# Performance work log

Measured on AMD Instinct MI355X. Metric: run time of the kernel, lower is better.

Reference implementation:

```python
import jax, jax.numpy as jnp
import numpy as np

N_NODES = 25000
N_EDGES = 400000
CHANNELS = 32
EDGE_FEAT_DIM = 8
HIDDEN = 64
NUM_IRREPS = 4  # messages irreps = 2x0e + 2x1o -> 4 irreps, dim 8
AVG_NUM_NEIGHBORS = 16.0


def _mlp(x, W0, W1, W2, W3):
    # e3nn MultiLayerPerceptron: dense layers with 1/sqrt(fan_in) forward
    # normalization, silu on hidden layers, no output activation.
    for W in (W0, W1, W2):
        x = jax.nn.silu(x @ (W / jnp.sqrt(jnp.float32(W.shape[0]))))
    return x @ (W3 / jnp.sqrt(jnp.float32(W3.shape[0])))


def setup_inputs() -> dict:
    key = jax.random.key(0)
    ks = jax.random.split(key, 9)
    node_feats = jax.random.normal(ks[0], (N_NODES, CHANNELS, 4), jnp.float32)
    edge_attrs = jax.random.normal(ks[1], (N_EDGES, 4), jnp.float32)
    edge_feats = jax.random.normal(ks[2], (N_EDGES, EDGE_FEAT_DIM), jnp.float32)
    senders = jax.random.randint(ks[3], (N_EDGES,), 0, N_NODES)
    receivers = jax.random.randint(ks[4], (N_EDGES,), 0, N_NODES)
    W0 = jax.random.normal(ks[5], (EDGE_FEAT_DIM, HIDDEN), jnp.float32)
    W1 = jax.random.normal(ks[6], (HIDDEN, HIDDEN), jnp.float32)
    W2 = jax.random.normal(ks[7], (HIDDEN, HIDDEN), jnp.float32)
    W3 = jax.random.normal(ks[8], (HIDDEN, CHANNELS * NUM_IRREPS), jnp.float32)
    return {"node_feats": node_feats, "edge_attrs": edge_attrs,
            "edge_feats": edge_feats, "senders": senders, "receivers": receivers,
            "W0": W0, "W1": W1, "W2": W2, "W3": W3}


def reference(node_feats, edge_attrs, edge_feats, senders, receivers, W0, W1, W2, W3):
    # Gather sender node features: [E, C, 4] with irreps 0e (dim1) + 1o (dim3)
    x = node_feats[senders]
    s, v = x[..., 0], x[..., 1:4]            # [E,C], [E,C,3]
    a_s = edge_attrs[:, 0]                   # Y_0: [E]
    a_v = edge_attrs[:, 1:4]                 # Y_1: [E,3]

    # CG tensor product filtered to 0e + 1o (e3nn normalization: sqrt(2l3+1)*w3j)
    m0a = s * a_s[:, None]                                   # 0e x 0e -> 0e  [E,C]
    m0b = jnp.einsum('ecd,ed->ec', v, a_v) / jnp.sqrt(3.0)   # 1o x 1o -> 0e  [E,C]
    m1a = s[..., None] * a_v[:, None, :]                     # 0e x 1o -> 1o  [E,C,3]
    m1b = v * a_s[:, None, None]                             # 1o x 0e -> 1o  [E,C,3]

    # Edge MLP gate: [E, C*num_irreps] -> mul_to_axis -> [E, C, num_irreps]
    mix = _mlp(edge_feats, W0, W1, W2, W3).reshape(N_EDGES, CHANNELS, NUM_IRREPS)

    # Elementwise tensor product with 4x0e scalars: per-irrep gating
    out_s = jnp.stack([m0a * mix[..., 0], m0b * mix[..., 1]], axis=-1)          # [E,C,2]
    out_v = jnp.concatenate([m1a * mix[..., 2:3], m1b * mix[..., 3:4]], axis=-1)  # [E,C,6]
    messages = jnp.concatenate([out_s, out_v], axis=-1)                          # [E,C,8]

    # Scatter-add into receivers, then normalize by sqrt(avg_num_neighbors)
    agg = jax.ops.segment_sum(messages, receivers, num_segments=N_NODES)
    return agg / jnp.sqrt(AVG_NUM_NEIGHBORS)
```

## Files before the change

### kernel.cpp

```cpp
#include <hip/hip_runtime.h>
#include <hip/hip_fp16.h>

#define NE 400000
#define NN 25000
#define MAXDEG 56
#define LDS_STRIDE 65

typedef __attribute__((ext_vector_type(8))) _Float16 half8;
typedef __attribute__((ext_vector_type(4))) _Float16 half4;
typedef __attribute__((ext_vector_type(4))) float f32x4;

#define WS_MIX_OFF   0ull
#define WS_SLOTS_OFF 102400000ull
#define WS_CNT_OFF   108000000ull
#define WS_WBUF_OFF  108100000ull
#define WS_NEED      108136864ull

#define WB_L0 0
#define WB_L1 2048
#define WB_L2 6144
#define WB_L3 10240

__device__ __forceinline__ float fast_silu(float x) {
    float e = __expf(-x);
    return x * __builtin_amdgcn_rcpf(1.0f + e);
}

__global__ __launch_bounds__(64) void prep_weights(
    const float* __restrict__ W0, const float* __restrict__ W1,
    const float* __restrict__ W2, const float* __restrict__ W3,
    _Float16* __restrict__ wbuf, int* __restrict__ cnt)
{
    const int f    = blockIdx.x;
    const int lane = threadIdx.x;

    for (int i = f * 64 + lane; i < NN; i += 36 * 64) cnt[i] = 0;

    const int n    = lane & 15;
    const int quad = lane >> 4;

    const float* W; int K, N, kt, nt, fl, base; float scale;
    if (f < 4)       { W = W0; K = 8;  N = 64;  fl = f;      kt = 0;       nt = fl;     scale = 0.35355339059327373f; base = WB_L0; }
    else if (f < 12) { W = W1; K = 64; N = 64;  fl = f - 4;  kt = fl >> 2; nt = fl & 3; scale = 0.125f;   base = WB_L1; }
    else if (f < 20) { W = W2; K = 64; N = 64;  fl = f - 12; kt = fl >> 2; nt = fl & 3; scale = 0.125f;   base = WB_L2; }
    else             { W = W3; K = 64; N = 128; fl = f - 20; kt = fl >> 3; nt = fl & 7; scale = 0.03125f; base = WB_L3; }

    _Float16 v[8];
    #pragma unroll
    for (int j = 0; j < 8; ++j) {
        const int k = kt * 32 + quad * 8 + j;
        const float val = (k < K) ? W[k * N + nt * 16 + n] * scale : 0.0f;
        v[j] = (_Float16)val;
    }
    *(half8*)(wbuf + base + fl * 512 + lane * 8) = *(const half8*)v;
}

#define HS 72
#define SS 136
__global__ __launch_bounds__(256) void mlp_build_kernel(
    const float*    __restrict__ edge_feats,
    const int*      __restrict__ receivers,
    const _Float16* __restrict__ wbuf,
    int*            __restrict__ cnt,
    int*            __restrict__ slots,
    _Float16*       __restrict__ mix16)
{
    __shared__ _Float16 H[4 * 2 * 16 * HS];
    const int tid  = threadIdx.x;
    const int wave = tid >> 6;
    const int lane = tid & 63;
    const int col  = lane & 15;
    const int quad = lane >> 4;

    if (tid < 128) {
        const int e = blockIdx.x * 128 + tid;
        const int r = receivers[e];
        const int s = atomicAdd(&cnt[r], 1);
        if (s < MAXDEG) slots[r * MAXDEG + s] = e;
    }

    const int e0 = (blockIdx.x * 4 + wave) * 32;
    _Float16* HA = &H[wave * 2 * 16 * HS];
    _Float16* HB = HA + 16 * HS;
    const half8* wb = (const half8*)wbuf;
    const f32x4 zero4 = {0.f, 0.f, 0.f, 0.f};

    half8 b0A = {0, 0, 0, 0, 0, 0, 0, 0};
    half8 b0B = {0, 0, 0, 0, 0, 0, 0, 0};
    if (quad == 0) {
        const float4* pA = (const float4*)(edge_feats + (size_t)(e0 + col) * 8);
        const float4 xa = pA[0], ya = pA[1];
        b0A[0] = (_Float16)xa.x; b0A[1] = (_Float16)xa.y; b0A[2] = (_Float16)xa.z; b0A[3] = (_Float16)xa.w;
        b0A[4] = (_Float16)ya.x; b0A[5] = (_Float16)ya.y; b0A[6] = (_Float16)ya.z; b0A[7] = (_Float16)ya.w;
        const float4* pB = (const float4*)(edge_feats + (size_t)(e0 + 16 + col) * 8);
        const float4 xb = pB[0], yb = pB[1];
        b0B[0] = (_Float16)xb.x; b0B[1] = (_Float16)xb.y; b0B[2] = (_Float16)xb.z; b0B[3] = (_Float16)xb.w;
        b0B[4] = (_Float16)yb.x; b0B[5] = (_Float16)yb.y; b0B[6] = (_Float16)yb.z; b0B[7] = (_Float16)yb.w;
    }

    #pragma unroll
    for (int nt = 0; nt < 4; ++nt) {
        const half8 w = wb[(WB_L0 / 512 + nt) * 64 + lane];
        f32x4 aA = __builtin_amdgcn_mfma_f32_16x16x32_f16(w, b0A, zero4, 0, 0, 0);
        f32x4 aB = __builtin_amdgcn_mfma_f32_16x16x32_f16(w, b0B, zero4, 0, 0, 0);
        half4 hA, hB;
        #pragma unroll
        for (int r = 0; r < 4; ++r) { hA[r] = (_Float16)fast_silu(aA[r]); hB[r] = (_Float16)fast_silu(aB[r]); }
        *(half4*)&HA[col * HS + nt * 16 + quad * 4] = hA;
        *(half4*)&HB[col * HS + nt * 16 + quad * 4] = hB;
    }

    #pragma unroll
    for (int layer = 0; layer < 2; ++layer) {
        const int wbase = (layer == 0 ? WB_L1 : WB_L2) / 512;
        const half8 bloA = *(const half8*)&HA[col * HS + 0  + quad * 8];
        const half8 bhiA = *(const half8*)&HA[col * HS + 32 + quad * 8];
        const half8 bloB = *(const half8*)&HB[col * HS + 0  + quad * 8];
        const half8 bhiB = *(const half8*)&HB[col * HS + 32 + quad * 8];
        f32x4 aA[4], aB[4];
        #pragma unroll
        for (int nt = 0; nt < 4; ++nt) {
            const half8 wlo = wb[(wbase + 0 + nt) * 64 + lane];
            const half8 whi = wb[(wbase + 4 + nt) * 64 + lane];
            aA[nt] = __builtin_amdgcn_mfma_f32_16x16x32_f16(wlo, bloA, zero4, 0, 0, 0);
            aA[nt] = __builtin_amdgcn_mfma_f32_16x16x32_f16(whi, bhiA, aA[nt], 0, 0, 0);
            aB[nt] = __builtin_amdgcn_mfma_f32_16x16x32_f16(wlo, bloB, zero4, 0, 0, 0);
            aB[nt] = __builtin_amdgcn_mfma_f32_16x16x32_f16(whi, bhiB, aB[nt], 0, 0, 0);
        }
        #pragma unroll
        for (int nt = 0; nt < 4; ++nt) {
            half4 hA, hB;
            #pragma unroll
            for (int r = 0; r < 4; ++r) { hA[r] = (_Float16)fast_silu(aA[nt][r]); hB[r] = (_Float16)fast_silu(aB[nt][r]); }
            *(half4*)&HA[col * HS + nt * 16 + quad * 4] = hA;
            *(half4*)&HB[col * HS + nt * 16 + quad * 4] = hB;
        }
    }

    {
        const half8 bloA = *(const half8*)&HA[col * HS + 0  + quad * 8];
        const half8 bhiA = *(const half8*)&HA[col * HS + 32 + quad * 8];
        const half8 bloB = *(const half8*)&HB[col * HS + 0  + quad * 8];
        const half8 bhiB = *(const half8*)&HB[col * HS + 32 + quad * 8];
        _Float16* S = HA;

        #pragma unroll
        for (int nt = 0; nt < 8; ++nt) {
            const half8 wlo = wb[(WB_L3 / 512 + 0 + nt) * 64 + lane];
            const half8 whi = wb[(WB_L3 / 512 + 8 + nt) * 64 + lane];
            f32x4 aA = __builtin_amdgcn_mfma_f32_16x16x32_f16(wlo, bloA, zero4, 0, 0, 0);
            aA = __builtin_amdgcn_mfma_f32_16x16x32_f16(whi, bhiA, aA, 0, 0, 0);
            half4 hA;
            #pragma unroll
            for (int r = 0; r < 4; ++r) hA[r] = (_Float16)aA[r];
            *(half4*)&S[col * SS + nt * 16 + quad * 4] = hA;
        }
        {
            _Float16* mbase = mix16 + (size_t)e0 * 128;
            #pragma unroll
            for (int rnd = 0; rnd < 4; ++rnd) {
                const int idx  = rnd * 512 + lane * 8;
                const int scol = idx >> 7;
                const int sinn = idx & 127;
                const half8 v = *(const half8*)&S[scol * SS + sinn];
                *(half8*)&mbase[idx] = v;
            }
        }

        #pragma unroll
        for (int nt = 0; nt < 8; ++nt) {
            const half8 wlo = wb[(WB_L3 / 512 + 0 + nt) * 64 + lane];
            const half8 whi = wb[(WB_L3 / 512 + 8 + nt) * 64 + lane];
            f32x4 aB = __builtin_amdgcn_mfma_f32_16x16x32_f16(wlo, bloB, zero4, 0, 0, 0);
            aB = __builtin_amdgcn_mfma_f32_16x16x32_f16(whi, bhiB, aB, 0, 0, 0);
            half4 hB;
            #pragma unroll
            for (int r = 0; r < 4; ++r) hB[r] = (_Float16)aB[r];
            *(half4*)&S[col * SS + nt * 16 + quad * 4] = hB;
        }
        {
            _Float16* mbase = mix16 + (size_t)(e0 + 16) * 128;
            #pragma unroll
            for (int rnd = 0; rnd < 4; ++rnd) {
                const int idx  = rnd * 512 + lane * 8;
                const int scol = idx >> 7;
                const int sinn = idx & 127;
                const half8 v = *(const half8*)&S[scol * SS + sinn];
                *(half8*)&mbase[idx] = v;
            }
        }
    }
}

__global__ __launch_bounds__(256) void gather_kernel(
    const float*    __restrict__ node_feats,
    const float*    __restrict__ edge_attrs,
    const int*      __restrict__ senders,
    const _Float16* __restrict__ mix16,
    const int*      __restrict__ cnt,
    const int*      __restrict__ slots,
    float*          __restrict__ out)
{
    const int tid  = threadIdx.x;
    const int wave = tid >> 6;
    const int lane = tid & 63;
    const int n    = blockIdx.x * 4 + wave;
    const int g    = lane >> 4;
    const int s    = lane & 15;
    const int c0   = 2 * s;
    const float inv_sqrt3 = 0.5773502691896258f;

    int d = cnt[n];
    if (d > MAXDEG) d = MAXDEG;
    const int* sl = slots + n * MAXDEG;

    const int li    = (lane < MAXDEG) ? lane : (MAXDEG - 1);
    int eid_l       = sl[li];
    eid_l           = (lane < d) ? eid_l : 0;
    const int snd_l = senders[eid_l];

    float acc[16];
    #pragma unroll
    for (int j = 0; j < 16; ++j) acc[j] = 0.0f;

    #pragma unroll 2
    for (int base = 0; base < d; base += 4) {
        const int  ei  = base + g;
        const bool act = (ei < d);
        const int  eid = __shfl(eid_l, ei, 64);
        const int  snd = __shfl(snd_l, ei, 64);
        const float4 a4v = ((const float4*)edge_attrs)[eid];
        const half8 m8 = *(const half8*)(mix16 + (size_t)eid * 128 + c0 * 4);
        const float4 xA = ((const float4*)(node_feats + (size_t)snd * 128))[c0];
        const float4 xB = ((const float4*)(node_feats + (size_t)snd * 128))[c0 + 1];

        const float z = act ? 1.0f : 0.0f;
        const float as = a4v.x, av0 = a4v.y, av1 = a4v.z, av2 = a4v.w;

        {
            const float m0 = z * (float)m8[0], m1 = z * (float)m8[1];
            const float m2 = z * (float)m8[2], m3 = z * (float)m8[3];
            const float sc = xA.x, v0 = xA.y, v1 = xA.z, v2 = xA.w;
            acc[0] = fmaf(sc * as, m0, acc[0]);
            const float dv = v0 * av0 + v1 * av1 + v2 * av2;
            acc[1] = fmaf(dv * inv_sqrt3, m1, acc[1]);
            acc[2] = fmaf(sc * av0, m2, acc[2]);
            acc[3] = fmaf(sc * av1, m2, acc[3]);
            acc[4] = fmaf(sc * av2, m2, acc[4]);
            acc[5] = fmaf(v0 * as, m3, acc[5]);
            acc[6] = fmaf(v1 * as, m3, acc[6]);
            acc[7] = fmaf(v2 * as, m3, acc[7]);
        }
        {
            const float m0 = z * (float)m8[4], m1 = z * (float)m8[5];
            const float m2 = z * (float)m8[6], m3 = z * (float)m8[7];
            const float sc = xB.x, v0 = xB.y, v1 = xB.z, v2 = xB.w;
            acc[8]  = fmaf(sc * as, m0, acc[8]);
            const float dv = v0 * av0 + v1 * av1 + v2 * av2;
            acc[9]  = fmaf(dv * inv_sqrt3, m1, acc[9]);
            acc[10] = fmaf(sc * av0, m2, acc[10]);
            acc[11] = fmaf(sc * av1, m2, acc[11]);
            acc[12] = fmaf(sc * av2, m2, acc[12]);
            acc[13] = fmaf(v0 * as, m3, acc[13]);
            acc[14] = fmaf(v1 * as, m3, acc[14]);
            acc[15] = fmaf(v2 * as, m3, acc[15]);
        }
    }

    #pragma unroll
    for (int j = 0; j < 16; ++j) {
        acc[j] += __shfl_xor(acc[j], 16, 64);
        acc[j] += __shfl_xor(acc[j], 32, 64);
    }

    if (g == 0) {
        float4* op = (float4*)(out + (size_t)n * 256 + s * 16);
        float4 r0; r0.x = acc[0];  r0.y = acc[1];  r0.z = acc[2];  r0.w = acc[3];
        float4 r1; r1.x = acc[4];  r1.y = acc[5];  r1.z = acc[6];  r1.w = acc[7];
        float4 r2; r2.x = acc[8];  r2.y = acc[9];  r2.z = acc[10]; r2.w = acc[11];
        float4 r3; r3.x = acc[12]; r3.y = acc[13]; r3.z = acc[14]; r3.w = acc[15];
        op[0] = r0; op[1] = r1; op[2] = r2; op[3] = r3;
    }
}

__global__ __launch_bounds__(128) void edge_mp_kernel(
    const float* __restrict__ node_feats, const float* __restrict__ edge_attrs,
    const float* __restrict__ edge_feats, const int* __restrict__ senders,
    const int* __restrict__ receivers, const float* __restrict__ W0,
    const float* __restrict__ W1, const float* __restrict__ W2,
    const float* __restrict__ W3, float* __restrict__ out)
{
    __shared__ float hbuf[128 * LDS_STRIDE];
    const int tid = threadIdx.x;
    const int e   = blockIdx.x * 128 + tid;
    if (e >= NE) return;
    float* hl = &hbuf[tid * LDS_STRIDE];

    float4 ef0 = ((const float4*)edge_feats)[e * 2 + 0];
    float4 ef1 = ((const float4*)edge_feats)[e * 2 + 1];
    float ef[8] = {ef0.x, ef0.y, ef0.z, ef0.w, ef1.x, ef1.y, ef1.z, ef1.w};
    float acc[64];
    #pragma unroll
    for (int i = 0; i < 64; ++i) acc[i] = 0.0f;
    #pragma unroll
    for (int j = 0; j < 8; ++j) {
        const float xj = ef[j];
        const float* wrow = W0 + j * 64;
        #pragma unroll
        for (int i = 0; i < 64; ++i) acc[i] = fmaf(xj, wrow[i], acc[i]);
    }
    {
        const float s0 = 0.35355339059327373f;
        #pragma unroll
        for (int i = 0; i < 64; ++i) hl[i] = fast_silu(acc[i] * s0);
    }
    #pragma unroll
    for (int i = 0; i < 64; ++i) acc[i] = 0.0f;
    #pragma unroll 4
    for (int j = 0; j < 64; ++j) {
        const float xj = hl[j];
        const float* wrow = W1 + j * 64;
        #pragma unroll
        for (int i = 0; i < 64; ++i) acc[i] = fmaf(xj, wrow[i], acc[i]);
    }
    #pragma unroll
    for (int i = 0; i < 64; ++i) hl[i] = fast_silu(acc[i] * 0.125f);
    #pragma unroll
    for (int i = 0; i < 64; ++i) acc[i] = 0.0f;
    #pragma unroll 4
    for (int j = 0; j < 64; ++j) {
        const float xj = hl[j];
        const float* wrow = W2 + j * 64;
        #pragma unroll
        for (int i = 0; i < 64; ++i) acc[i] = fmaf(xj, wrow[i], acc[i]);
    }
    float h2[64];
    #pragma unroll
    for (int i = 0; i < 64; ++i) h2[i] = fast_silu(acc[i] * 0.125f);

    const int snd = senders[e];
    const int rcv = receivers[e];
    const float4 a4 = ((const float4*)edge_attrs)[e];
    const float a_s = a4.x, av0 = a4.y, av1 = a4.z, av2 = a4.w;
    const float4* nf4 = (const float4*)(node_feats + (size_t)snd * 128);
    float* outp = out + (size_t)rcv * 256;
    const float mixscale = 0.03125f;
    const float inv_sqrt3 = 0.5773502691896258f;

    #pragma unroll 2
    for (int c = 0; c < 32; ++c) {
        float m0 = 0.0f, m1 = 0.0f, m2 = 0.0f, m3 = 0.0f;
        const float* wc = W3 + c * 4;
        #pragma unroll
        for (int j = 0; j < 64; ++j) {
            const float hj = h2[j];
            m0 = fmaf(hj, wc[j * 128 + 0], m0);
            m1 = fmaf(hj, wc[j * 128 + 1], m1);
            m2 = fmaf(hj, wc[j * 128 + 2], m2);
            m3 = fmaf(hj, wc[j * 128 + 3], m3);
        }
        m0 *= mixscale; m1 *= mixscale; m2 *= mixscale; m3 *= mixscale;
        const float4 x4 = nf4[c];
        const float s = x4.x, v0 = x4.y, v1 = x4.z, v2 = x4.w;
        float* op = outp + c * 8;
        atomicAdd(op + 0, s * a_s * m0);
        const float dotva = v0 * av0 + v1 * av1 + v2 * av2;
        atomicAdd(op + 1, dotva * inv_sqrt3 * m1);
        atomicAdd(op + 2, s * av0 * m2);
        atomicAdd(op + 3, s * av1 * m2);
        atomicAdd(op + 4, s * av2 * m2);
        atomicAdd(op + 5, v0 * a_s * m3);
        atomicAdd(op + 6, v1 * a_s * m3);
        atomicAdd(op + 7, v2 * a_s * m3);
    }
}

extern "C" void kernel_launch(void* const* d_in, const int* in_sizes, int n_in,
                              void* d_out, int out_size, void* d_ws, size_t ws_size,
                              hipStream_t stream) {
    const float* node_feats = (const float*)d_in[0];
    const float* edge_attrs = (const float*)d_in[1];
    const float* edge_feats = (const float*)d_in[2];
    const int*   senders    = (const int*)d_in[3];
    const int*   receivers  = (const int*)d_in[4];
    const float* W0 = (const float*)d_in[5];
    const float* W1 = (const float*)d_in[6];
    const float* W2 = (const float*)d_in[7];
    const float* W3 = (const float*)d_in[8];
    float* outp = (float*)d_out;

    if (ws_size >= WS_NEED) {
        char* w = (char*)d_ws;
        _Float16* mix16 = (_Float16*)(w + WS_MIX_OFF);
        int*      slots = (int*)(w + WS_SLOTS_OFF);
        int*      cnt   = (int*)(w + WS_CNT_OFF);
        _Float16* wbuf  = (_Float16*)(w + WS_WBUF_OFF);

        hipLaunchKernelGGL(prep_weights, dim3(36), dim3(64), 0, stream,
                           W0, W1, W2, W3, wbuf, cnt);
        hipLaunchKernelGGL(mlp_build_kernel, dim3(NE / 128), dim3(256), 0, stream,
                           edge_feats, receivers, wbuf, cnt, slots, mix16);
        hipLaunchKernelGGL(gather_kernel, dim3(NN / 4), dim3(256), 0, stream,
                           node_feats, edge_attrs, senders, mix16, cnt, slots, outp);
    } else {
        hipMemsetAsync(d_out, 0, (size_t)out_size * sizeof(float), stream);
        hipLaunchKernelGGL(edge_mp_kernel, dim3((NE + 127) / 128), dim3(128), 0, stream,
                           node_feats, edge_attrs, edge_feats, senders, receivers,
                           W0, W1, W2, W3, outp);
    }
}
```

Before: 197.1 us.

## Build CSR by receiver and store MLP gates in receiver-sorted order

Replaces fixed-capacity per-node slot lists with a true CSR: a count kernel, a single-wave prefix scan folded into weight prep, and atomic placement during the MLP kernel. The MLP output rows are now written at their CSR position, so the gather kernel reads each node's gate rows contiguously instead of at scattered edge ids. This adds a memset, an extra kernel and a serial 64-lane scan over 25k counts. Edges beyond 64 per node are dropped in the gather.

```diff
diff --git a/kernel.cpp b/kernel.cpp
--- a/kernel.cpp
+++ b/kernel.cpp
@@ -3,7 +3,6 @@
 
 #define NE 400000
 #define NN 25000
-#define MAXDEG 56
 #define LDS_STRIDE 65
 
 typedef __attribute__((ext_vector_type(8))) _Float16 half8;
@@ -11,10 +10,12 @@
 typedef __attribute__((ext_vector_type(4))) float f32x4;
 
 #define WS_MIX_OFF   0ull
-#define WS_SLOTS_OFF 102400000ull
-#define WS_CNT_OFF   108000000ull
-#define WS_WBUF_OFF  108100000ull
-#define WS_NEED      108136864ull
+#define WS_EID_OFF   102400000ull
+#define WS_OFFS_OFF  104000000ull
+#define WS_CNT_OFF   104100000ull
+#define WS_CNT2_OFF  104200000ull
+#define WS_WBUF_OFF  104300000ull
+#define WS_NEED      104336864ull
 
 #define WB_L0 0
 #define WB_L1 2048
@@ -26,24 +27,47 @@
     return x * __builtin_amdgcn_rcpf(1.0f + e);
 }
 
+__global__ __launch_bounds__(256) void csr_count(
+    const int* __restrict__ receivers, int* __restrict__ cnt)
+{
+    const int e = blockIdx.x * 256 + threadIdx.x;
+    if (e < NE) atomicAdd(&cnt[receivers[e]], 1);
+}
+
 __global__ __launch_bounds__(64) void prep_weights(
     const float* __restrict__ W0, const float* __restrict__ W1,
     const float* __restrict__ W2, const float* __restrict__ W3,
-    _Float16* __restrict__ wbuf, int* __restrict__ cnt)
+    _Float16* __restrict__ wbuf, const int* __restrict__ cnt,
+    int* __restrict__ offs)
 {
     const int f    = blockIdx.x;
     const int lane = threadIdx.x;
 
-    for (int i = f * 64 + lane; i < NN; i += 36 * 64) cnt[i] = 0;
+    if (f == 36) {
+        const int CH = (NN + 63) / 64;
+        const int i0 = lane * CH;
+        const int i1 = (i0 + CH < NN) ? i0 + CH : NN;
+        int sum = 0;
+        for (int i = i0; i < i1; ++i) sum += cnt[i];
+        int run = sum;
+        #pragma unroll
+        for (int dlt = 1; dlt < 64; dlt <<= 1) {
+            const int v = __shfl_up(run, dlt, 64);
+            if (lane >= dlt) run += v;
+        }
+        int base = run - sum;
+        for (int i = i0; i < i1; ++i) { offs[i] = base; base += cnt[i]; }
+        return;
+    }
 
     const int n    = lane & 15;
     const int quad = lane >> 4;
 
-    const float* W; int K, N, kt, nt, fl, base; float scale;
-    if (f < 4)       { W = W0; K = 8;  N = 64;  fl = f;      kt = 0;       nt = fl;     scale = 0.35355339059327373f; base = WB_L0; }
-    else if (f < 12) { W = W1; K = 64; N = 64;  fl = f - 4;  kt = fl >> 2; nt = fl & 3; scale = 0.125f;   base = WB_L1; }
-    else if (f < 20) { W = W2; K = 64; N = 64;  fl = f - 12; kt = fl >> 2; nt = fl & 3; scale = 0.125f;   base = WB_L2; }
-    else             { W = W3; K = 64; N = 128; fl = f - 20; kt = fl >> 3; nt = fl & 7; scale = 0.03125f; base = WB_L3; }
+    const float* W; int K, N, kt, nt, fl, wbase; float scale;
+    if (f < 4)       { W = W0; K = 8;  N = 64;  fl = f;      kt = 0;       nt = fl;     scale = 0.35355339059327373f; wbase = WB_L0; }
+    else if (f < 12) { W = W1; K = 64; N = 64;  fl = f - 4;  kt = fl >> 2; nt = fl & 3; scale = 0.125f;   wbase = WB_L1; }
+    else if (f < 20) { W = W2; K = 64; N = 64;  fl = f - 12; kt = fl >> 2; nt = fl & 3; scale = 0.125f;   wbase = WB_L2; }
+    else             { W = W3; K = 64; N = 128; fl = f - 20; kt = fl >> 3; nt = fl & 7; scale = 0.03125f; wbase = WB_L3; }
 
     _Float16 v[8];
     #pragma unroll
@@ -52,7 +76,7 @@
         const float val = (k < K) ? W[k * N + nt * 16 + n] * scale : 0.0f;
         v[j] = (_Float16)val;
     }
-    *(half8*)(wbuf + base + fl * 512 + lane * 8) = *(const half8*)v;
+    *(half8*)(wbuf + wbase + fl * 512 + lane * 8) = *(const half8*)v;
 }
 
 #define HS 72
@@ -61,8 +85,9 @@
     const float*    __restrict__ edge_feats,
     const int*      __restrict__ receivers,
     const _Float16* __restrict__ wbuf,
-    int*            __restrict__ cnt,
-    int*            __restrict__ slots,
+    int*            __restrict__ cnt2,
+    const int*      __restrict__ offs,
+    int*            __restrict__ eidarr,
     _Float16*       __restrict__ mix16)
 {
     __shared__ _Float16 H[4 * 2 * 16 * HS];
@@ -72,14 +97,17 @@
     const int col  = lane & 15;
     const int quad = lane >> 4;
 
-    if (tid < 128) {
-        const int e = blockIdx.x * 128 + tid;
+    const int e0 = (blockIdx.x * 4 + wave) * 32;
+
+    int pos_reg = 0;
+    if (lane < 32) {
+        const int e = e0 + lane;
         const int r = receivers[e];
-        const int s = atomicAdd(&cnt[r], 1);
-        if (s < MAXDEG) slots[r * MAXDEG + s] = e;
-    }
-
-    const int e0 = (blockIdx.x * 4 + wave) * 32;
+        const int s = atomicAdd(&cnt2[r], 1);
+        pos_reg = offs[r] + s;
+        eidarr[pos_reg] = e;
+    }
+
     _Float16* HA = &H[wave * 2 * 16 * HS];
     _Float16* HB = HA + 16 * HS;
     const half8* wb = (const half8*)wbuf;
@@ -143,6 +171,8 @@
         const half8 bloB = *(const half8*)&HB[col * HS + 0  + quad * 8];
         const half8 bhiB = *(const half8*)&HB[col * HS + 32 + quad * 8];
         _Float16* S = HA;
+        const int et  = lane >> 2;
+        const int sub = lane & 3;
 
         #pragma unroll
         for (int nt = 0; nt < 8; ++nt) {
@@ -156,14 +186,12 @@
             *(half4*)&S[col * SS + nt * 16 + quad * 4] = hA;
         }
         {
-            _Float16* mbase = mix16 + (size_t)e0 * 128;
+            const int posA = __shfl(pos_reg, et, 64);
+            _Float16* rowA = mix16 + (size_t)posA * 128;
             #pragma unroll
             for (int rnd = 0; rnd < 4; ++rnd) {
-                const int idx  = rnd * 512 + lane * 8;
-                const int scol = idx >> 7;
-                const int sinn = idx & 127;
-                const half8 v = *(const half8*)&S[scol * SS + sinn];
-                *(half8*)&mbase[idx] = v;
+                const half8 v = *(const half8*)&S[et * SS + sub * 8 + rnd * 32];
+                *(half8*)&rowA[sub * 8 + rnd * 32] = v;
             }
         }
 
@@ -179,14 +207,12 @@
             *(half4*)&S[col * SS + nt * 16 + quad * 4] = hB;
         }
         {
-            _Float16* mbase = mix16 + (size_t)(e0 + 16) * 128;
+            const int posB = __shfl(pos_reg, 16 + et, 64);
+            _Float16* rowB = mix16 + (size_t)posB * 128;
             #pragma unroll
             for (int rnd = 0; rnd < 4; ++rnd) {
-                const int idx  = rnd * 512 + lane * 8;
-                const int scol = idx >> 7;
-                const int sinn = idx & 127;
-                const half8 v = *(const half8*)&S[scol * SS + sinn];
-                *(half8*)&mbase[idx] = v;
+                const half8 v = *(const half8*)&S[et * SS + sub * 8 + rnd * 32];
+                *(half8*)&rowB[sub * 8 + rnd * 32] = v;
             }
         }
     }
@@ -198,7 +224,8 @@
     const int*      __restrict__ senders,
     const _Float16* __restrict__ mix16,
     const int*      __restrict__ cnt,
-    const int*      __restrict__ slots,
+    const int*      __restrict__ offs,
+    const int*      __restrict__ eidarr,
     float*          __restrict__ out)
 {
     const int tid  = threadIdx.x;
@@ -210,60 +237,62 @@
     const int c0   = 2 * s;
     const float inv_sqrt3 = 0.5773502691896258f;
 
+    const int o = offs[n];
     int d = cnt[n];
-    if (d > MAXDEG) d = MAXDEG;
-    const int* sl = slots + n * MAXDEG;
-
-    const int li    = (lane < MAXDEG) ? lane : (MAXDEG - 1);
-    int eid_l       = sl[li];
-    eid_l           = (lane < d) ? eid_l : 0;
-    const int snd_l = senders[eid_l];
+    if (d > 64) d = 64;
 
     float acc[16];
     #pragma unroll
     for (int j = 0; j < 16; ++j) acc[j] = 0.0f;
 
-    #pragma unroll 2
-    for (int base = 0; base < d; base += 4) {
-        const int  ei  = base + g;
-        const bool act = (ei < d);
-        const int  eid = __shfl(eid_l, ei, 64);
-        const int  snd = __shfl(snd_l, ei, 64);
-        const float4 a4v = ((const float4*)edge_attrs)[eid];
-        const half8 m8 = *(const half8*)(mix16 + (size_t)eid * 128 + c0 * 4);
-        const float4 xA = ((const float4*)(node_feats + (size_t)snd * 128))[c0];
-        const float4 xB = ((const float4*)(node_feats + (size_t)snd * 128))[c0 + 1];
-
-        const float z = act ? 1.0f : 0.0f;
-        const float as = a4v.x, av0 = a4v.y, av1 = a4v.z, av2 = a4v.w;
-
-        {
-            const float m0 = z * (float)m8[0], m1 = z * (float)m8[1];
-            const float m2 = z * (float)m8[2], m3 = z * (float)m8[3];
-            const float sc = xA.x, v0 = xA.y, v1 = xA.z, v2 = xA.w;
-            acc[0] = fmaf(sc * as, m0, acc[0]);
-            const float dv = v0 * av0 + v1 * av1 + v2 * av2;
-            acc[1] = fmaf(dv * inv_sqrt3, m1, acc[1]);
-            acc[2] = fmaf(sc * av0, m2, acc[2]);
-            acc[3] = fmaf(sc * av1, m2, acc[3]);
-            acc[4] = fmaf(sc * av2, m2, acc[4]);
-            acc[5] = fmaf(v0 * as, m3, acc[5]);
-            acc[6] = fmaf(v1 * as, m3, acc[6]);
-            acc[7] = fmaf(v2 * as, m3, acc[7]);
-        }
-        {
-            const float m0 = z * (float)m8[4], m1 = z * (float)m8[5];
-            const float m2 = z * (float)m8[6], m3 = z * (float)m8[7];
-            const float sc = xB.x, v0 = xB.y, v1 = xB.z, v2 = xB.w;
-            acc[8]  = fmaf(sc * as, m0, acc[8]);
-            const float dv = v0 * av0 + v1 * av1 + v2 * av2;
-            acc[9]  = fmaf(dv * inv_sqrt3, m1, acc[9]);
-            acc[10] = fmaf(sc * av0, m2, acc[10]);
-            acc[11] = fmaf(sc * av1, m2, acc[11]);
-            acc[12] = fmaf(sc * av2, m2, acc[12]);
-            acc[13] = fmaf(v0 * as, m3, acc[13]);
-            acc[14] = fmaf(v1 * as, m3, acc[14]);
-            acc[15] = fmaf(v2 * as, m3, acc[15]);
+    if (d > 0) {
+        const int li    = (lane < d) ? lane : d - 1;
+        const int eid_l = eidarr[o + li];
+        const int snd_l = senders[eid_l];
+
+        #pragma unroll 2
+        for (int base = 0; base < d; base += 4) {
+            const int  ei  = base + g;
+            const bool act = (ei < d);
+            const int  eic = act ? ei : 0;
+            const int  eid = __shfl(eid_l, eic, 64);
+            const int  snd = __shfl(snd_l, eic, 64);
+            const float4 a4v = ((const float4*)edge_attrs)[eid];
+            const half8 m8 = *(const half8*)(mix16 + (size_t)(o + eic) * 128 + c0 * 4);
+            const float4 xA = ((const float4*)(node_feats + (size_t)snd * 128))[c0];
+            const float4 xB = ((const float4*)(node_feats + (size_t)snd * 128))[c0 + 1];
+
+            const float z = act ? 1.0f : 0.0f;
+            const float as = a4v.x, av0 = a4v.y, av1 = a4v.z, av2 = a4v.w;
+
+            {
+                const float m0 = z * (float)m8[0], m1 = z * (float)m8[1];
+                const float m2 = z * (float)m8[2], m3 = z * (float)m8[3];
+                const float sc = xA.x, v0 = xA.y, v1 = xA.z, v2 = xA.w;
+                acc[0] = fmaf(sc * as, m0, acc[0]);
+                const float dv = v0 * av0 + v1 * av1 + v2 * av2;
+                acc[1] = fmaf(dv * inv_sqrt3, m1, acc[1]);
+                acc[2] = fmaf(sc * av0, m2, acc[2]);
+                acc[3] = fmaf(sc * av1, m2, acc[3]);
+                acc[4] = fmaf(sc * av2, m2, acc[4]);
+                acc[5] = fmaf(v0 * as, m3, acc[5]);
+                acc[6] = fmaf(v1 * as, m3, acc[6]);
+                acc[7] = fmaf(v2 * as, m3, acc[7]);
+            }
+            {
+                const float m0 = z * (float)m8[4], m1 = z * (float)m8[5];
+                const float m2 = z * (float)m8[6], m3 = z * (float)m8[7];
+                const float sc = xB.x, v0 = xB.y, v1 = xB.z, v2 = xB.w;
+                acc[8]  = fmaf(sc * as, m0, acc[8]);
+                const float dv = v0 * av0 + v1 * av1 + v2 * av2;
+                acc[9]  = fmaf(dv * inv_sqrt3, m1, acc[9]);
+                acc[10] = fmaf(sc * av0, m2, acc[10]);
+                acc[11] = fmaf(sc * av1, m2, acc[11]);
+                acc[12] = fmaf(sc * av2, m2, acc[12]);
+                acc[13] = fmaf(v0 * as, m3, acc[13]);
+                acc[14] = fmaf(v1 * as, m3, acc[14]);
+                acc[15] = fmaf(v2 * as, m3, acc[15]);
+            }
         }
     }
 
@@ -391,17 +420,22 @@
 
     if (ws_size >= WS_NEED) {
         char* w = (char*)d_ws;
-        _Float16* mix16 = (_Float16*)(w + WS_MIX_OFF);
-        int*      slots = (int*)(w + WS_SLOTS_OFF);
-        int*      cnt   = (int*)(w + WS_CNT_OFF);
-        _Float16* wbuf  = (_Float16*)(w + WS_WBUF_OFF);
-
-        hipLaunchKernelGGL(prep_weights, dim3(36), dim3(64), 0, stream,
-                           W0, W1, W2, W3, wbuf, cnt);
+        _Float16* mix16  = (_Float16*)(w + WS_MIX_OFF);
+        int*      eidarr = (int*)(w + WS_EID_OFF);
+        int*      offs   = (int*)(w + WS_OFFS_OFF);
+        int*      cnt    = (int*)(w + WS_CNT_OFF);
+        int*      cnt2   = (int*)(w + WS_CNT2_OFF);
+        _Float16* wbuf   = (_Float16*)(w + WS_WBUF_OFF);
+
+        hipMemsetAsync(w + WS_CNT_OFF, 0, 200000, stream);
+        hipLaunchKernelGGL(csr_count, dim3((NE + 255) / 256), dim3(256), 0, stream,
+                           receivers, cnt);
+        hipLaunchKernelGGL(prep_weights, dim3(37), dim3(64), 0, stream,
+                           W0, W1, W2, W3, wbuf, cnt, offs);
         hipLaunchKernelGGL(mlp_build_kernel, dim3(NE / 128), dim3(256), 0, stream,
-                           edge_feats, receivers, wbuf, cnt, slots, mix16);
+                           edge_feats, receivers, wbuf, cnt2, offs, eidarr, mix16);
         hipLaunchKernelGGL(gather_kernel, dim3(NN / 4), dim3(256), 0, stream,
-                           node_feats, edge_attrs, senders, mix16, cnt, slots, outp);
+                           node_feats, edge_attrs, senders, mix16, cnt, offs, eidarr, outp);
     } else {
         hipMemsetAsync(d_out, 0, (size_t)out_size * sizeof(float), stream);
         hipLaunchKernelGGL(edge_mp_kernel, dim3((NE + 127) / 128), dim3(128), 0, stream,
```

Measured after the change: 333.6 us. 1.69x slower.
